# Optimization experiments

Measured on AMD Instinct MI355X. Metric: run time of the kernel, lower is better.

The kernel has to match this reference:

```python
import jax, jax.numpy as jnp
import numpy as np

DELTA_V = 0.2
DELTA_D = 1.2


def safe_norm(x, axis):
    # L2 norm with zero (sub)gradient at 0, matching torch.norm backward convention.
    s = jnp.sum(x * x, axis=axis)
    nz = (s > 0).astype(x.dtype)
    return jnp.sqrt(jnp.where(s > 0, s, 1.0)) * nz


def setup_inputs() -> dict:
    key = jax.random.key(0)
    k1, k2 = jax.random.split(key)
    preds = jax.random.normal(k1, (4, 8, 280, 640), dtype=jnp.float32)
    targets = jax.random.randint(k2, (4, 280, 640), 0, 6, dtype=jnp.int32)
    return {"preds": preds, "targets": targets, "group_num": 5}


def reference(preds, targets, group_num):
    # preds: (N, C, H, W) embedding; targets: (N, H, W) lane ids (0 = background)
    N, C, H, W = preds.shape
    P = H * W
    mask = (targets > 0).reshape(N, P)                      # lane points
    g = jnp.where(mask, targets.reshape(N, P) - 1, 0)       # group labels 0..G-1
    # one-hot group membership, zeroed on background (N, P, G)
    gt = jax.nn.one_hot(g, group_num, dtype=preds.dtype) * mask[:, :, None].astype(preds.dtype)
    point_num = gt.sum(1)                                   # (N, G)
    has_point = (point_num > 0).astype(preds.dtype)         # (N, G)
    n_groups = has_point.sum(1)                             # (N,)

    pred = preds.transpose(0, 2, 3, 1).reshape(N, P, C)     # (N, P, C)
    # per-group centers via segmented reduce expressed as einsum
    center = jnp.einsum('npc,npg->ngc', pred, gt) / (point_num[:, :, None] + 1e-5)  # (N, G, C)

    # variance term: distance of each point to every group center, masked by membership
    diff = pred[:, :, None, :] - center[:, None, :, :]      # (N, P, G, C)
    d_v = safe_norm(diff, axis=3)                           # (N, P, G)
    loss_var = (jnp.clip(d_v - DELTA_V, 0.0) ** 2 * gt).sum((1, 2)) / n_groups
    loss_var = loss_var.mean()

    # distance term: pairwise center distances; rows masked by has_point (diagonal included, as in torch)
    cdiff = center[:, None, :, :] - center[:, :, None, :]   # (N, G, G, C): [n,i,j] = c_j - c_i
    dmat = safe_norm(cdiff, axis=3)                         # (N, G, G)
    loss_dist = (jnp.clip(DELTA_D - dmat, 0.0) ** 2 * has_point[:, :, None]).sum((1, 2))
    loss_dist = loss_dist / jnp.clip(n_groups * (n_groups - 1.0), 1.0)
    loss_dist = loss_dist.mean()

    # regularization: squared sum of center coordinates for groups that have points
    loss_reg = ((center.sum(-1) ** 2) * has_point).sum() * 0.001

    # matches torch return dict: {'dist': loss_dist, 'var': loss_var * 0.01, 'reg': loss_reg}
    return jnp.stack([loss_dist, loss_var * 0.01, loss_reg])
```

## Files before the change

kernel.cpp:

```cpp
#include <hip/hip_runtime.h>


#define P_TOTAL (280 * 640)
#define NBATCH 4
#define GN 5
#define CC 8
#define NVAL (GN * CC + GN)
#define LPAD 47

#define WAVE_RED(x)                          \
  do {                                       \
    x += __shfl_xor(x, 32, 64);              \
    x += __shfl_xor(x, 16, 64);              \
    x += __shfl_xor(x, 8, 64);               \
    x += __shfl_xor(x, 4, 64);               \
    x += __shfl_xor(x, 2, 64);               \
    x += __shfl_xor(x, 1, 64);               \
  } while (0)

__global__ __launch_bounds__(256) void k_accum(const float* __restrict__ preds,
                                               const int* __restrict__ targets,
                                               float* __restrict__ ws) {
  const int n = blockIdx.y;
  const int tid = threadIdx.x;
  const int p4 = (blockIdx.x * 256 + tid) * 4;

  const float* pn = preds + (size_t)n * CC * P_TOTAL;
  const int* tn = targets + (size_t)n * P_TOTAL;

  float acc[GN][CC];
  float cnt[GN];
#pragma unroll
  for (int g = 0; g < GN; ++g) {
    cnt[g] = 0.0f;
#pragma unroll
    for (int c = 0; c < CC; ++c) acc[g][c] = 0.0f;
  }

  {
    int4 t4 = *reinterpret_cast<const int4*>(tn + p4);
    int t[4] = {t4.x, t4.y, t4.z, t4.w};
    float4 v4[CC];
#pragma unroll
    for (int c = 0; c < CC; ++c)
      v4[c] = *reinterpret_cast<const float4*>(pn + (size_t)c * P_TOTAL + p4);
    float v[CC][4];
#pragma unroll
    for (int c = 0; c < CC; ++c) {
      v[c][0] = v4[c].x; v[c][1] = v4[c].y; v[c][2] = v4[c].z; v[c][3] = v4[c].w;
    }
#pragma unroll
    for (int s = 0; s < 4; ++s) {
#pragma unroll
      for (int g = 0; g < GN; ++g) {
        float m = (t[s] == g + 1) ? 1.0f : 0.0f;
        cnt[g] += m;
#pragma unroll
        for (int c = 0; c < CC; ++c) acc[g][c] = fmaf(m, v[c][s], acc[g][c]);
      }
    }
  }

  __shared__ float buf[256][LPAD];
  __shared__ float part4[NVAL][4];
#pragma unroll
  for (int g = 0; g < GN; ++g) {
#pragma unroll
    for (int c = 0; c < CC; ++c) buf[tid][g * CC + c] = acc[g][c];
    buf[tid][GN * CC + g] = cnt[g];
  }
  __syncthreads();

  if (tid < NVAL * 4) {
    const int k = tid >> 2;
    const int part = tid & 3;
    float s = 0.0f;
#pragma unroll
    for (int r = 0; r < 64; ++r) s += buf[(r << 2) + part][k];
    part4[k][part] = s;
  }
  __syncthreads();

  if (tid < NVAL) {
    float s = part4[tid][0] + part4[tid][1] + part4[tid][2] + part4[tid][3];
    if (tid < GN * CC)
      atomicAdd(&ws[n * (GN * CC) + tid], s);
    else
      atomicAdd(&ws[NBATCH * GN * CC + n * GN + (tid - GN * CC)], s);
  }
}

__global__ __launch_bounds__(256) void k_var(const float* __restrict__ preds,
                                             const int* __restrict__ targets,
                                             float* __restrict__ ws) {
  const int n = blockIdx.y;
  const int tid = threadIdx.x;

  __shared__ float center[GN][CC];
  if (tid < GN * CC) {
    int g = tid >> 3;
    center[g][tid & 7] =
        ws[n * (GN * CC) + tid] / (ws[NBATCH * GN * CC + n * GN + g] + 1e-5f);
  }
  __syncthreads();

  const float* pn = preds + (size_t)n * CC * P_TOTAL;
  const int* tn = targets + (size_t)n * P_TOTAL;
  const int p4 = (blockIdx.x * 256 + tid) * 4;

  float accv = 0.0f;
  {
    int4 t4 = *reinterpret_cast<const int4*>(tn + p4);
    int t[4] = {t4.x, t4.y, t4.z, t4.w};
    float4 v4[CC];
#pragma unroll
    for (int c = 0; c < CC; ++c)
      v4[c] = *reinterpret_cast<const float4*>(pn + (size_t)c * P_TOTAL + p4);
    float v[CC][4];
#pragma unroll
    for (int c = 0; c < CC; ++c) {
      v[c][0] = v4[c].x; v[c][1] = v4[c].y; v[c][2] = v4[c].z; v[c][3] = v4[c].w;
    }
#pragma unroll
    for (int s = 0; s < 4; ++s) {
      int ts = t[s];
      if (ts > 0) {
        int g = ts - 1;
        float ss = 0.0f;
#pragma unroll
        for (int c = 0; c < CC; ++c) {
          float d = v[c][s] - center[g][c];
          ss = fmaf(d, d, ss);
        }
        float dn = sqrtf(ss);
        float cl = fmaxf(dn - 0.2f, 0.0f);
        accv = fmaf(cl, cl, accv);
      }
    }
  }

  WAVE_RED(accv);
  __shared__ float red[4];
  const int lane = tid & 63;
  const int wv = tid >> 6;
  if (lane == 0) red[wv] = accv;
  __syncthreads();
  if (tid == 0) {
    float s = red[0] + red[1] + red[2] + red[3];
    atomicAdd(&ws[NBATCH * GN * CC + NBATCH * GN + n], s);
  }
}

__global__ __launch_bounds__(64) void k_final(const float* __restrict__ ws,
                                              float* __restrict__ out) {
  const int tid = threadIdx.x;
  __shared__ float sdist[NBATCH], svar[NBATCH], sreg[NBATCH];
  if (tid < NBATCH) {
    const int n = tid;
    float center[GN][CC];
    float has[GN];
    float ng = 0.0f;
#pragma unroll
    for (int g = 0; g < GN; ++g) {
      float c_ = ws[NBATCH * GN * CC + n * GN + g];
      has[g] = (c_ > 0.0f) ? 1.0f : 0.0f;
      ng += has[g];
#pragma unroll
      for (int c = 0; c < CC; ++c)
        center[g][c] = ws[n * (GN * CC) + g * CC + c] / (c_ + 1e-5f);
    }
    float lv = ws[NBATCH * GN * CC + NBATCH * GN + n] / ng;
    float ld = 0.0f;
#pragma unroll
    for (int i = 0; i < GN; ++i) {
#pragma unroll
      for (int j = 0; j < GN; ++j) {
        float ss = 0.0f;
#pragma unroll
        for (int c = 0; c < CC; ++c) {
          float d = center[j][c] - center[i][c];
          ss = fmaf(d, d, ss);
        }
        float dn = (ss > 0.0f) ? sqrtf(ss) : 0.0f;
        float cl = fmaxf(1.2f - dn, 0.0f);
        ld += cl * cl * has[i];
      }
    }
    ld /= fmaxf(ng * (ng - 1.0f), 1.0f);
    float lr = 0.0f;
#pragma unroll
    for (int g = 0; g < GN; ++g) {
      float cs = 0.0f;
#pragma unroll
      for (int c = 0; c < CC; ++c) cs += center[g][c];
      lr += cs * cs * has[g];
    }
    sdist[n] = ld;
    svar[n] = lv;
    sreg[n] = lr;
  }
  __syncthreads();
  if (tid == 0) {
    float d = 0.0f, v = 0.0f, r = 0.0f;
#pragma unroll
    for (int n = 0; n < NBATCH; ++n) { d += sdist[n]; v += svar[n]; r += sreg[n]; }
    out[0] = d * 0.25f;
    out[1] = v * 0.25f * 0.01f;
    out[2] = r * 0.001f;
  }
}

extern "C" void kernel_launch(void* const* d_in, const int* in_sizes, int n_in,
                              void* d_out, int out_size, void* d_ws, size_t ws_size,
                              hipStream_t stream) {
  const float* preds = (const float*)d_in[0];
  const int* targets = (const int*)d_in[1];
  float* out = (float*)d_out;
  float* ws = (float*)d_ws;

  hipMemsetAsync(ws, 0, (NBATCH * GN * CC + NBATCH * GN + NBATCH) * sizeof(float),
                 stream);

  dim3 grid(P_TOTAL / (256 * 4), NBATCH);
  k_accum<<<grid, 256, 0, stream>>>(preds, targets, ws);
  k_var<<<grid, 256, 0, stream>>>(preds, targets, ws);
  k_final<<<1, 64, 0, stream>>>(ws, out);
}
```

Measured before the change: 96.87 us.

## Replace atomics and memset with per-block partials, fuse final reduction via last-block

Each accumulation block now writes its partial sums to its own workspace slot instead of doing global atomicAdds, so the memset launch is no longer needed. Every k_var block re-reduces the 175 partials for its batch to rebuild the centers. The separate final kernel is folded into k_var using a threadfence plus atomic counter, so only the last block to finish computes the outputs. This removes two launches and the atomic contention, at the cost of redundant partial reads in every k_var block and a serial tail in the last block.

```diff
diff --git a/kernel.cpp b/kernel.cpp
--- a/kernel.cpp
+++ b/kernel.cpp
@@ -7,6 +7,10 @@
 #define CC 8
 #define NVAL (GN * CC + GN)
 #define LPAD 47
+#define NBX 175
+#define NBLK (NBX * NBATCH)
+#define WS_VP (NBLK * NVAL)
+#define WS_CNT (WS_VP + NBLK)
 
 #define WAVE_RED(x)                          \
   do {                                       \
@@ -22,8 +26,11 @@
                                                const int* __restrict__ targets,
                                                float* __restrict__ ws) {
   const int n = blockIdx.y;
+  const int b = n * NBX + blockIdx.x;
   const int tid = threadIdx.x;
   const int p4 = (blockIdx.x * 256 + tid) * 4;
+
+  if (b == 0 && tid == 0) ((int*)ws)[WS_CNT] = 0;
 
   const float* pn = preds + (size_t)n * CC * P_TOTAL;
   const int* tn = targets + (size_t)n * P_TOTAL;
@@ -83,24 +90,30 @@
 
   if (tid < NVAL) {
     float s = part4[tid][0] + part4[tid][1] + part4[tid][2] + part4[tid][3];
-    if (tid < GN * CC)
-      atomicAdd(&ws[n * (GN * CC) + tid], s);
-    else
-      atomicAdd(&ws[NBATCH * GN * CC + n * GN + (tid - GN * CC)], s);
+    ws[b * NVAL + tid] = s;
   }
 }
 
 __global__ __launch_bounds__(256) void k_var(const float* __restrict__ preds,
                                              const int* __restrict__ targets,
-                                             float* __restrict__ ws) {
+                                             float* __restrict__ ws,
+                                             float* __restrict__ out) {
   const int n = blockIdx.y;
+  const int b = n * NBX + blockIdx.x;
   const int tid = threadIdx.x;
 
+  __shared__ float asum[NVAL];
   __shared__ float center[GN][CC];
+  if (tid < NVAL) {
+    float s = 0.0f;
+    const float* base = ws + n * NBX * NVAL + tid;
+    for (int r = 0; r < NBX; ++r) s += base[r * NVAL];
+    asum[tid] = s;
+  }
+  __syncthreads();
   if (tid < GN * CC) {
     int g = tid >> 3;
-    center[g][tid & 7] =
-        ws[n * (GN * CC) + tid] / (ws[NBATCH * GN * CC + n * GN + g] + 1e-5f);
+    center[g][tid & 7] = asum[g * CC + (tid & 7)] / (asum[GN * CC + g] + 1e-5f);
   }
   __syncthreads();
 
@@ -141,35 +154,57 @@
 
   WAVE_RED(accv);
   __shared__ float red[4];
+  __shared__ int isLast;
   const int lane = tid & 63;
   const int wv = tid >> 6;
   if (lane == 0) red[wv] = accv;
   __syncthreads();
   if (tid == 0) {
     float s = red[0] + red[1] + red[2] + red[3];
-    atomicAdd(&ws[NBATCH * GN * CC + NBATCH * GN + n], s);
-  }
-}
-
-__global__ __launch_bounds__(64) void k_final(const float* __restrict__ ws,
-                                              float* __restrict__ out) {
-  const int tid = threadIdx.x;
-  __shared__ float sdist[NBATCH], svar[NBATCH], sreg[NBATCH];
+    ws[WS_VP + b] = s;
+    __threadfence();
+    int old = atomicAdd((int*)ws + WS_CNT, 1);
+    isLast = (old == NBLK - 1) ? 1 : 0;
+  }
+  __syncthreads();
+  if (!isLast) return;
+
+  __threadfence();
+
+  __shared__ float fsum[NBATCH][NVAL];
+  __shared__ float vsum[NBATCH];
+  __shared__ float res[NBATCH][3];
+  if (tid < NBATCH * NVAL) {
+    const int n2 = tid / NVAL;
+    const int k = tid % NVAL;
+    float s = 0.0f;
+    const float* base = ws + n2 * NBX * NVAL + k;
+    for (int r = 0; r < NBX; ++r) s += base[r * NVAL];
+    fsum[n2][k] = s;
+  }
+  {
+    float s = 0.0f;
+    for (int j = lane; j < NBX; j += 64) s += ws[WS_VP + wv * NBX + j];
+    WAVE_RED(s);
+    if (lane == 0) vsum[wv] = s;
+  }
+  __syncthreads();
+
   if (tid < NBATCH) {
-    const int n = tid;
-    float center[GN][CC];
+    const int nn = tid;
+    float cen[GN][CC];
     float has[GN];
     float ng = 0.0f;
 #pragma unroll
     for (int g = 0; g < GN; ++g) {
-      float c_ = ws[NBATCH * GN * CC + n * GN + g];
+      float c_ = fsum[nn][GN * CC + g];
       has[g] = (c_ > 0.0f) ? 1.0f : 0.0f;
       ng += has[g];
 #pragma unroll
       for (int c = 0; c < CC; ++c)
-        center[g][c] = ws[n * (GN * CC) + g * CC + c] / (c_ + 1e-5f);
-    }
-    float lv = ws[NBATCH * GN * CC + NBATCH * GN + n] / ng;
+        cen[g][c] = fsum[nn][g * CC + c] / (c_ + 1e-5f);
+    }
+    float lv = vsum[nn] / ng;
     float ld = 0.0f;
 #pragma unroll
     for (int i = 0; i < GN; ++i) {
@@ -178,7 +213,7 @@
         float ss = 0.0f;
 #pragma unroll
         for (int c = 0; c < CC; ++c) {
-          float d = center[j][c] - center[i][c];
+          float d = cen[j][c] - cen[i][c];
           ss = fmaf(d, d, ss);
         }
         float dn = (ss > 0.0f) ? sqrtf(ss) : 0.0f;
@@ -192,18 +227,20 @@
     for (int g = 0; g < GN; ++g) {
       float cs = 0.0f;
 #pragma unroll
-      for (int c = 0; c < CC; ++c) cs += center[g][c];
+      for (int c = 0; c < CC; ++c) cs += cen[g][c];
       lr += cs * cs * has[g];
     }
-    sdist[n] = ld;
-    svar[n] = lv;
-    sreg[n] = lr;
+    res[nn][0] = ld;
+    res[nn][1] = lv;
+    res[nn][2] = lr;
   }
   __syncthreads();
   if (tid == 0) {
     float d = 0.0f, v = 0.0f, r = 0.0f;
 #pragma unroll
-    for (int n = 0; n < NBATCH; ++n) { d += sdist[n]; v += svar[n]; r += sreg[n]; }
+    for (int nn = 0; nn < NBATCH; ++nn) {
+      d += res[nn][0]; v += res[nn][1]; r += res[nn][2];
+    }
     out[0] = d * 0.25f;
     out[1] = v * 0.25f * 0.01f;
     out[2] = r * 0.001f;
@@ -218,11 +255,7 @@
   float* out = (float*)d_out;
   float* ws = (float*)d_ws;
 
-  hipMemsetAsync(ws, 0, (NBATCH * GN * CC + NBATCH * GN + NBATCH) * sizeof(float),
-                 stream);
-
-  dim3 grid(P_TOTAL / (256 * 4), NBATCH);
+  dim3 grid(NBX, NBATCH);
   k_accum<<<grid, 256, 0, stream>>>(preds, targets, ws);
-  k_var<<<grid, 256, 0, stream>>>(preds, targets, ws);
-  k_final<<<1, 64, 0, stream>>>(ws, out);
+  k_var<<<grid, 256, 0, stream>>>(preds, targets, ws, out);
 }
```

Result: slower. 105.2 us (+8.6%).
